# Performance work log

Measured on AMD Instinct MI355X. Metric: run time of the kernel, lower is better.

Reference implementation:

```python
import jax, jax.numpy as jnp
import numpy as np

EPS = 1e-5

def _inst_norm(x):
    # x: (B,C,H,W); torch .var(dim=2) is unbiased (ddof=1) over HW
    B, C, H, W = x.shape
    xf = x.reshape(B, C, H * W)
    mean = xf.mean(axis=2, keepdims=True)
    var = xf.var(axis=2, ddof=1, keepdims=True) + EPS
    return ((xf - mean) / jnp.sqrt(var)).reshape(B, C, H, W)

def _conv1x1(x, w, b):
    # (out,in) weight applied channelwise
    return jnp.einsum('oc,bchw->bohw', w, x) + b[None, :, None, None]

def setup_inputs() -> dict:
    key = jax.random.key(0)
    ks = jax.random.split(key, 10)
    B, C, H, W = 4, 512, 64, 64
    s = 1.0 / np.sqrt(C)
    return {
        'x_fcc': jax.random.normal(ks[0], (B, C, H, W), jnp.float32),
        'x_fss': jax.random.normal(ks[1], (B, C, H, W), jnp.float32),
        'w1': jax.random.normal(ks[2], (C, C), jnp.float32) * s,
        'b1': jax.random.normal(ks[3], (C,), jnp.float32) * 0.01,
        'w2': jax.random.normal(ks[4], (C, C), jnp.float32) * s,
        'b2': jax.random.normal(ks[5], (C,), jnp.float32) * 0.01,
        'w3': jax.random.normal(ks[6], (C, C), jnp.float32) * s,
        'b3': jax.random.normal(ks[7], (C,), jnp.float32) * 0.01,
        'wrs': jax.random.normal(ks[8], (C, C), jnp.float32) * s,
        'brs': jax.random.normal(ks[9], (C,), jnp.float32) * 0.01,
    }

def reference(x_fcc, x_fss, w1, b1, w2, b2, w3, b3, wrs, brs):
    Bc, Cc, Hc, Wc = x_fcc.shape
    Bs, Cs, Hs, Ws = x_fss.shape
    q = _conv1x1(_inst_norm(x_fcc), w1, b1).reshape(Bc, Cc, Hc * Wc)
    k = _conv1x1(_inst_norm(x_fss), w2, b2).reshape(Bs, Cs, Hs * Ws)
    v = _conv1x1(x_fss, w3, b3).reshape(Bc, Cs, Hs * Ws)
    # attention: (B, HWc, HWs), softmax over style positions
    scores = jnp.einsum('bcq,bck->bqk', q, k)
    A = jax.nn.softmax(scores, axis=-1)
    # aggregate style values per content position: (B, C, HWc)
    frs = jnp.einsum('bck,bqk->bcq', v, A).reshape(x_fcc.shape)
    frs = _conv1x1(frs, wrs, brs)
    return frs + x_fcc
```

## Files before the change

kernel.cpp:

```cpp
#include <hip/hip_runtime.h>
#include <hip/hip_bf16.h>


typedef _Float16 f16_t;
typedef _Float16 f16x8 __attribute__((ext_vector_type(8)));
typedef float f32x4 __attribute__((ext_vector_type(4)));

#define C_DIM 512
#define HW_DIM 4096
#define NBATCH 4
#define CHW (512L * 4096L)

__device__ inline f32x4 mfma_f16(f16x8 a, f16x8 b, f32x4 c) {
    return __builtin_amdgcn_mfma_f32_16x16x32_f16(a, b, c, 0, 0, 0);
}

__device__ inline void g2l16(const f16_t* g, f16_t* l) {
    auto gp = (const __attribute__((address_space(1))) uint32_t*)(uintptr_t)g;
    auto lp = (__attribute__((address_space(3))) uint32_t*)(uint32_t)(uintptr_t)l;
    __builtin_amdgcn_global_load_lds(gp, lp, 16, 0, 0);
}

template<int N> __device__ inline void vmwait() {
    static_assert(N == 0 || N == 6, "add vmcnt case");
    if constexpr (N == 0) asm volatile("s_waitcnt vmcnt(0)" ::: "memory");
    else                  asm volatile("s_waitcnt vmcnt(6)" ::: "memory");
}

__device__ inline void barrier_mem() {
    asm volatile("s_barrier" ::: "memory");
    __builtin_amdgcn_sched_barrier(0);
}

__global__ __launch_bounds__(256) void stats_kernel(
    const float* __restrict__ xc, const float* __restrict__ xs,
    float* __restrict__ meanc, float* __restrict__ rstdc,
    float* __restrict__ means, float* __restrict__ rstds)
{
    int id = blockIdx.x;
    int bc = id & 2047;
    const float4* x = (const float4*)((id < 2048 ? xc : xs) + (size_t)bc * HW_DIM);
    int tid = threadIdx.x;
    float s = 0.f, ss = 0.f;
#pragma unroll
    for (int i = 0; i < 4; i++) {
        float4 v = x[tid + (i << 8)];
        s += v.x + v.y + v.z + v.w;
        ss += v.x * v.x + v.y * v.y + v.z * v.z + v.w * v.w;
    }
#pragma unroll
    for (int o = 32; o; o >>= 1) { s += __shfl_down(s, o); ss += __shfl_down(ss, o); }
    __shared__ float red[8];
    if ((tid & 63) == 0) { red[(tid >> 6) * 2] = s; red[(tid >> 6) * 2 + 1] = ss; }
    __syncthreads();
    if (tid == 0) {
        s  = red[0] + red[2] + red[4] + red[6];
        ss = red[1] + red[3] + red[5] + red[7];
        float mean = s * (1.0f / 4096.0f);
        float var  = (ss - 4096.0f * mean * mean) * (1.0f / 4095.0f);
        float rstd = rsqrtf(var + 1e-5f);
        if (id < 2048) { meanc[bc] = mean; rstdc[bc] = rstd; }
        else           { means[bc] = mean; rstds[bc] = rstd; }
    }
}

__global__ __launch_bounds__(256) void pack_w4_kernel(
    const float* __restrict__ w0, const float* __restrict__ w1,
    const float* __restrict__ w2, const float* __restrict__ w3,
    f16_t* __restrict__ h0, f16_t* __restrict__ h1,
    f16_t* __restrict__ h2, f16_t* __restrict__ h3,
    const float* __restrict__ bb0, const float* __restrict__ bb1,
    const float* __restrict__ bb2, const float* __restrict__ bb3,
    float* __restrict__ biasws)
{
    int which = blockIdx.y;
    const float* w = which == 0 ? w0 : which == 1 ? w1 : which == 2 ? w2 : w3;
    f16_t* h = which == 0 ? h0 : which == 1 ? h1 : which == 2 ? h2 : h3;
    const float* bs = which == 0 ? bb0 : which == 1 ? bb1 : which == 2 ? bb2 : bb3;
    int i = blockIdx.x * 256 + threadIdx.x;
    h[i] = (f16_t)w[i];
    if (i < C_DIM) biasws[which * C_DIM + i] = bs[i];
}

__global__ __launch_bounds__(256) void pack_T_kernel(
    const float* __restrict__ xc, const float* __restrict__ xs,
    const float* __restrict__ meanc, const float* __restrict__ rstdc,
    const float* __restrict__ means, const float* __restrict__ rstds,
    f16_t* __restrict__ ch, f16_t* __restrict__ sh, f16_t* __restrict__ sraw)
{
    __shared__ float tile[32][33];
    int z = blockIdx.z;
    int b = z & 3, src = z >> 2;
    const float* x    = (src == 0) ? xc : xs;
    const float* mean = (src == 0) ? meanc : means;
    const float* rstd = (src == 0) ? rstdc : rstds;

    int c0 = blockIdx.y * 32, p0 = blockIdx.x * 32;
    int tp = threadIdx.x & 31, tc8 = threadIdx.x >> 5;
    const float* xb = x + ((size_t)b * C_DIM + c0) * HW_DIM + p0;
#pragma unroll
    for (int it = 0; it < 4; it++) {
        int c = tc8 + it * 8;
        tile[c][tp] = xb[(size_t)c * HW_DIM + tp];
    }
    __syncthreads();
    int wc = threadIdx.x & 31, wp8 = threadIdx.x >> 5;
    float m = mean[b * C_DIM + c0 + wc];
    float r = rstd[b * C_DIM + c0 + wc];
    size_t obase = ((size_t)b * HW_DIM + p0) * C_DIM + c0;
    f16_t* ohb = ((src == 0) ? ch : sh) + obase;
    f16_t* srb = sraw + obase;
#pragma unroll
    for (int it = 0; it < 4; it++) {
        int p = wp8 + it * 8;
        float v = tile[wc][p];
        ohb[(size_t)p * C_DIM + wc] = (f16_t)((v - m) * r);
        if (src == 1) srb[(size_t)p * C_DIM + wc] = (f16_t)v;
    }
}

__global__ __launch_bounds__(256) void softmax_rows(
    const float* __restrict__ S, f16_t* __restrict__ P)
{
    int row = blockIdx.x;
    int tid = threadIdx.x;
    int wave = tid >> 6, lane = tid & 63;
    const float4* sr = (const float4*)(S + (size_t)row * HW_DIM);
    float4 v[4];
    float mx = -3.4e38f;
#pragma unroll
    for (int i = 0; i < 4; i++) {
        v[i] = sr[tid + (i << 8)];
        mx = fmaxf(mx, fmaxf(fmaxf(v[i].x, v[i].y), fmaxf(v[i].z, v[i].w)));
    }
#pragma unroll
    for (int o = 32; o; o >>= 1) mx = fmaxf(mx, __shfl_down(mx, o));
    __shared__ float red[4];
    if (lane == 0) red[wave] = mx;
    __syncthreads();
    mx = fmaxf(fmaxf(red[0], red[1]), fmaxf(red[2], red[3]));
    float sum = 0.f;
#pragma unroll
    for (int i = 0; i < 4; i++) {
        v[i].x = __expf(v[i].x - mx); v[i].y = __expf(v[i].y - mx);
        v[i].z = __expf(v[i].z - mx); v[i].w = __expf(v[i].w - mx);
        sum += v[i].x + v[i].y + v[i].z + v[i].w;
    }
#pragma unroll
    for (int o = 32; o; o >>= 1) sum += __shfl_down(sum, o);
    __syncthreads();
    if (lane == 0) red[wave] = sum;
    __syncthreads();
    sum = red[0] + red[1] + red[2] + red[3];
    float inv = 1.0f / sum;
    uint2* pr = (uint2*)(P + (size_t)row * HW_DIM);
#pragma unroll
    for (int i = 0; i < 4; i++) {
        union { uint2 u; f16_t h[4]; } o;
        o.h[0] = (f16_t)(v[i].x * inv); o.h[1] = (f16_t)(v[i].y * inv);
        o.h[2] = (f16_t)(v[i].z * inv); o.h[3] = (f16_t)(v[i].w * inv);
        pr[tid + (i << 8)] = o.u;
    }
}

__global__ __launch_bounds__(256) void reduce4_kernel(
    const float* __restrict__ part, f16_t* __restrict__ out)
{
    size_t i = (size_t)blockIdx.x * 256 + threadIdx.x;
    const float4* p0 = (const float4*)part;
    const float4* p1 = (const float4*)(part + CHW);
    const float4* p2 = (const float4*)(part + 2 * CHW);
    const float4* p3 = (const float4*)(part + 3 * CHW);
    float4 a = p0[i], b = p1[i], c = p2[i], d = p3[i];
    union { uint2 u; f16_t h[4]; } o;
    o.h[0] = (f16_t)(a.x + b.x + c.x + d.x);
    o.h[1] = (f16_t)(a.y + b.y + c.y + d.y);
    o.h[2] = (f16_t)(a.z + b.z + c.z + d.z);
    o.h[3] = (f16_t)(a.w + b.w + c.w + d.w);
    ((uint2*)out)[i] = o.u;
}

template<int EPI, bool QK, int NT, int CHX, int CHY>
__global__ __launch_bounds__(512, 2) void gemm256(
    const f16_t* __restrict__ Ah, const f16_t* __restrict__ Bh,
    void* __restrict__ Cout0, const float* __restrict__ bias,
    const float* __restrict__ resid,
    int lda, int ldc,
    long sAz, long sBz, long sCz, long sRz, long sAw, long sBw, long sCw)
{
    constexpr int AE = 256 * 64;
    constexpr int BE = 128 * 64;
    constexpr int BUFE = AE + BE;
    __shared__ __align__(16) f16_t smem[3 * BUFE];

    int bx, by, bz;
    {
        const int nbx = gridDim.x, nby = gridDim.y, nbz = gridDim.z;
        const int lin = ((int)blockIdx.z * nby + blockIdx.y) * nbx + blockIdx.x;
        const int nwg = nbx * nby * nbz;
        const int cpx = nwg >> 3;
        const int logical = (lin & 7) * cpx + (lin >> 3);
        constexpr int CHB = CHX * CHY;
        const int chunk  = logical / CHB;
        const int within = logical % CHB;
        const int cx = within % CHX, cy = within / CHX;
        const int chunks_x = nbx / CHX;
        const int chx = chunk % chunks_x;
        int tt = chunk / chunks_x;
        const int chunks_y = nby / CHY;
        bz = tt / chunks_y;
        by = (tt % chunks_y) * CHY + cy;
        bx = chx * CHX + cx;
    }

    const int tid  = threadIdx.x;
    const int wave = tid >> 6, lane = tid & 63;
    const int wm = (wave >> 2) * 128;
    const int wn = (wave & 3) * 32;
    const int fr = lane & 15;
    const int g16 = lane >> 4;
    const int key = fr & 7;

    const int z   = QK ? (bz & 3) : bz;
    const int sel = QK ? (bz >> 2) : 0;
    const f16_t* Az = Ah + (size_t)z * sAz + (size_t)sel * sAw;
    const f16_t* Bz = Bh + (size_t)z * sBz + (size_t)sel * sBw;
    const float* biasp = bias ? (bias + (QK ? sel * C_DIM : 0)) : nullptr;
    const long mBlock = (long)by * 256;
    const long nBlock = (long)bx * 128;

    const int srow8 = lane >> 3;
    const int gsrc  = ((lane & 7) ^ srow8) * 8;
    const f16_t* aSrc[4]; const f16_t* bSrc[2];
    int aDst[4], bDst[2];
#pragma unroll
    for (int q = 0; q < 4; q++) {
        int j = 4 * wave + q;
        aSrc[q] = Az + (size_t)(mBlock + 8 * j + srow8) * lda + gsrc;
        aDst[q] = j * 512;
    }
#pragma unroll
    for (int q = 0; q < 2; q++) {
        int j = 2 * wave + q;
        bSrc[q] = Bz + (size_t)(nBlock + 8 * j + srow8) * lda + gsrc;
        bDst[q] = AE + j * 512;
    }

    auto stageA = [&](int t) {
        f16_t* dst = smem + (t % 3) * BUFE;
        const int k0 = t * 64;
#pragma unroll
        for (int q = 0; q < 4; q++) g2l16(aSrc[q] + k0, dst + aDst[q]);
    };
    auto stageB = [&](int t) {
        f16_t* dst = smem + (t % 3) * BUFE;
        const int k0 = t * 64;
#pragma unroll
        for (int q = 0; q < 2; q++) g2l16(bSrc[q] + k0, dst + bDst[q]);
    };

    f32x4 acc[8][2];
#pragma unroll
    for (int i = 0; i < 8; i++)
#pragma unroll
        for (int j = 0; j < 2; j++) acc[i][j] = (f32x4){0.f, 0.f, 0.f, 0.f};

    stageA(0); stageB(0); stageA(1); stageB(1);
    vmwait<6>();
    barrier_mem();

#pragma unroll
    for (int t = 0; t < NT; ++t) {
        const f16_t* buf = smem + (t % 3) * BUFE;
#pragma unroll
        for (int ks = 0; ks < 2; ++ks) {
            f16x8 a[8], b[2];
            const int gr = ((ks * 4 + g16) ^ key) * 8;
#pragma unroll
            for (int j2 = 0; j2 < 2; j2++)
                b[j2] = *reinterpret_cast<const f16x8*>(
                    buf + AE + (wn + j2 * 16 + fr) * 64 + gr);
#pragma unroll
            for (int mi = 0; mi < 8; mi++)
                a[mi] = *reinterpret_cast<const f16x8*>(
                    buf + (wm + mi * 16 + fr) * 64 + gr);
            if (t + 2 < NT) { if (ks == 0) stageA(t + 2); else stageB(t + 2); }
            if (ks == 1) {
                if (t + 2 < NT)      vmwait<6>();
                else if (t + 1 < NT) vmwait<0>();
            }
            barrier_mem();
            __builtin_amdgcn_s_setprio(1);
#pragma unroll
            for (int mi = 0; mi < 8; mi++)
#pragma unroll
                for (int j2 = 0; j2 < 2; j2++)
                    acc[mi][j2] = mfma_f16(a[mi], b[j2], acc[mi][j2]);
            __builtin_amdgcn_s_setprio(0);
            barrier_mem();
        }
    }

    const int col  = lane & 15;
    const int rowq = (lane >> 4) * 4;
    const size_t cbase = (size_t)z * sCz + (size_t)sel * sCw;
#pragma unroll
    for (int mi = 0; mi < 8; mi++) {
        const long mb = mBlock + wm + mi * 16 + rowq;
        float bv[4];
#pragma unroll
        for (int r = 0; r < 4; r++) bv[r] = biasp ? biasp[mb + r] : 0.0f;
#pragma unroll
        for (int j2 = 0; j2 < 2; j2++) {
            const long n = nBlock + wn + j2 * 16 + col;
            float v[4];
#pragma unroll
            for (int r = 0; r < 4; r++) v[r] = acc[mi][j2][r] + bv[r];
            if constexpr (EPI == 0) {
                float* O = (float*)Cout0 + cbase;
                const float* R = resid ? (resid + (size_t)z * sRz) : nullptr;
#pragma unroll
                for (int r = 0; r < 4; r++) {
                    size_t off = (size_t)(mb + r) * ldc + n;
                    O[off] = v[r] + (R ? R[off] : 0.0f);
                }
            } else if constexpr (EPI == 1) {
                f16_t* O = (f16_t*)Cout0 + cbase;
#pragma unroll
                for (int r = 0; r < 4; r++) O[(size_t)(mb + r) * ldc + n] = (f16_t)v[r];
            } else if constexpr (EPI == 3) {
                alignas(8) f16_t h[4];
#pragma unroll
                for (int r = 0; r < 4; r++) h[r] = (f16_t)v[r];
                *reinterpret_cast<uint2*>((f16_t*)Cout0 + cbase + (size_t)n * ldc + mb)
                    = *reinterpret_cast<uint2*>(h);
            } else {
                alignas(16) float h[4];
#pragma unroll
                for (int r = 0; r < 4; r++) h[r] = v[r];
                *reinterpret_cast<float4*>((float*)Cout0 + cbase + (size_t)n * ldc + mb)
                    = *reinterpret_cast<float4*>(h);
            }
        }
    }
}

extern "C" void kernel_launch(void* const* d_in, const int* in_sizes, int n_in,
                              void* d_out, int out_size, void* d_ws, size_t ws_size,
                              hipStream_t stream)
{
    const float* x_fcc = (const float*)d_in[0];
    const float* x_fss = (const float*)d_in[1];
    const float* w1 = (const float*)d_in[2];
    const float* b1 = (const float*)d_in[3];
    const float* w2 = (const float*)d_in[4];
    const float* b2 = (const float*)d_in[5];
    const float* w3 = (const float*)d_in[6];
    const float* b3 = (const float*)d_in[7];
    const float* wrs = (const float*)d_in[8];
    const float* brs = (const float*)d_in[9];
    float* out = (float*)d_out;
    (void)n_in; (void)in_sizes; (void)out_size; (void)ws_size;

    char* base = (char*)d_ws;
    size_t off = 0;
    auto take = [&](size_t bytes) -> char* {
        char* p = base + off;
        off += (bytes + 255) & ~(size_t)255;
        return p;
    };
    const size_t WB = (size_t)C_DIM * C_DIM * sizeof(f16_t);
    const size_t TB = (size_t)NBATCH * CHW * sizeof(f16_t);
    const long  TBe = NBATCH * CHW;

    float* meanc = (float*)take(2048 * 4);
    float* rstdc = (float*)take(2048 * 4);
    float* means = (float*)take(2048 * 4);
    float* rstds = (float*)take(2048 * 4);
    float* biasws = (float*)take(4 * C_DIM * 4);
    f16_t* w1h = (f16_t*)take(WB);
    f16_t* w2h = (f16_t*)take(WB);
    f16_t* w3h = (f16_t*)take(WB);
    f16_t* wrh = (f16_t*)take(WB);
    f16_t* qT = (f16_t*)take(TB);
    f16_t* kT = (f16_t*)take(TB);
    f16_t* vh   = (f16_t*)take(TB);
    f16_t* frsT = (f16_t*)take(TB);
    char* packb = take(8 * TB);
    f16_t* xcT  = (f16_t*)(packb);
    f16_t* xsT  = (f16_t*)(packb + TB);
    f16_t* xsrT = (f16_t*)(packb + 2 * TB);
    float* Smat = (float*)(packb);
    f16_t* Pmat = (f16_t*)(packb + 4 * TB);
    float* Part = (float*)(packb + 6 * TB);

    dim3 blk(256);
    dim3 blk5(512);

    stats_kernel<<<dim3(4096), blk, 0, stream>>>(x_fcc, x_fss, meanc, rstdc, means, rstds);
    pack_w4_kernel<<<dim3(1024, 4), blk, 0, stream>>>(
        w1, w2, w3, wrs, w1h, w2h, w3h, wrh, b1, b2, b3, brs, biasws);
    pack_T_kernel<<<dim3(128, 16, 8), blk, 0, stream>>>(
        x_fcc, x_fss, meanc, rstdc, means, rstds, xcT, xsT, xsrT);
    gemm256<3, true, 8, 8, 2><<<dim3(32, 2, 8), blk5, 0, stream>>>(
        w1h, xcT, qT, biasws, nullptr, C_DIM, C_DIM,
        0L, CHW, CHW, 0L, (long)C_DIM * C_DIM, TBe, TBe);
    gemm256<1, false, 8, 8, 2><<<dim3(32, 2, 4), blk5, 0, stream>>>(
        w3h, xsrT, vh, biasws + 2 * C_DIM, nullptr, C_DIM, HW_DIM,
        0L, CHW, CHW, 0L, 0L, 0L, 0L);
    for (int b = 0; b < NBATCH; b++) {
        gemm256<0, false, 8, 8, 4><<<dim3(32, 16, 1), blk5, 0, stream>>>(
            qT + (size_t)b * CHW, kT + (size_t)b * CHW,
            Smat, nullptr, nullptr, C_DIM, HW_DIM,
            0L, 0L, 0L, 0L, 0L, 0L, 0L);
        softmax_rows<<<dim3(4096), blk, 0, stream>>>(Smat, Pmat);
        gemm256<4, false, 16, 8, 2><<<dim3(32, 2, 4), blk5, 0, stream>>>(
            vh + (size_t)b * CHW, Pmat,
            Part, nullptr, nullptr, HW_DIM, C_DIM,
            1024L, 1024L, CHW, 0L, 0L, 0L, 0L);
        reduce4_kernel<<<dim3(CHW / 1024), blk, 0, stream>>>(
            Part, frsT + (size_t)b * CHW);
    }
    gemm256<0, false, 8, 8, 2><<<dim3(32, 2, 4), blk5, 0, stream>>>(
        wrh, frsT, out, biasws + 3 * C_DIM, x_fcc, C_DIM, HW_DIM,
        0L, CHW, CHW, CHW, 0L, 0L, 0L);
}
```

Measured before the change: 533.4 us.

## Enlarge GEMM tile to 256x256 with double-buffered split-unit LDS staging

The GEMM kernel's output tile grows from 256x128 to 256x256. Each wave now computes 128x64 with 32 accumulators, and all launch grids are halved in x. The shared-memory pipeline changes from a 3-stage ring to a 2-stage double buffer split into four 128-row units, with finer-grained staging interleaved across half-steps. The aim is more MFMA work per byte loaded and fewer blocks, at the cost of more registers (which may cut occupancy below 2 blocks/CU), less pipeline depth, and fewer workgroups on the small GEMMs.

```diff
diff --git a/kernel.cpp b/kernel.cpp
--- a/kernel.cpp
+++ b/kernel.cpp
@@ -22,9 +22,9 @@
 }
 
 template<int N> __device__ inline void vmwait() {
-    static_assert(N == 0 || N == 6, "add vmcnt case");
+    static_assert(N == 0 || N == 2, "add vmcnt case");
     if constexpr (N == 0) asm volatile("s_waitcnt vmcnt(0)" ::: "memory");
-    else                  asm volatile("s_waitcnt vmcnt(6)" ::: "memory");
+    else                  asm volatile("s_waitcnt vmcnt(2)" ::: "memory");
 }
 
 __device__ inline void barrier_mem() {
@@ -188,10 +188,8 @@
     int lda, int ldc,
     long sAz, long sBz, long sCz, long sRz, long sAw, long sBw, long sCw)
 {
-    constexpr int AE = 256 * 64;
-    constexpr int BE = 128 * 64;
-    constexpr int BUFE = AE + BE;
-    __shared__ __align__(16) f16_t smem[3 * BUFE];
+    constexpr int UNIT = 128 * 64;
+    __shared__ __align__(16) f16_t smem[8 * UNIT];
 
     int bx, by, bz;
     {
@@ -216,10 +214,13 @@
     const int tid  = threadIdx.x;
     const int wave = tid >> 6, lane = tid & 63;
     const int wm = (wave >> 2) * 128;
-    const int wn = (wave & 3) * 32;
+    const int wn = (wave & 3) * 64;
     const int fr = lane & 15;
     const int g16 = lane >> 4;
     const int key = fr & 7;
+    const int ha  = wave >> 2;
+    const int hb  = wn >> 7;
+    const int rB  = wn - hb * 128;
 
     const int z   = QK ? (bz & 3) : bz;
     const int sel = QK ? (bz >> 2) : 0;
@@ -227,75 +228,84 @@
     const f16_t* Bz = Bh + (size_t)z * sBz + (size_t)sel * sBw;
     const float* biasp = bias ? (bias + (QK ? sel * C_DIM : 0)) : nullptr;
     const long mBlock = (long)by * 256;
-    const long nBlock = (long)bx * 128;
+    const long nBlock = (long)bx * 256;
 
     const int srow8 = lane >> 3;
     const int gsrc  = ((lane & 7) ^ srow8) * 8;
-    const f16_t* aSrc[4]; const f16_t* bSrc[2];
-    int aDst[4], bDst[2];
-#pragma unroll
-    for (int q = 0; q < 4; q++) {
-        int j = 4 * wave + q;
-        aSrc[q] = Az + (size_t)(mBlock + 8 * j + srow8) * lda + gsrc;
-        aDst[q] = j * 512;
-    }
-#pragma unroll
-    for (int q = 0; q < 2; q++) {
-        int j = 2 * wave + q;
-        bSrc[q] = Bz + (size_t)(nBlock + 8 * j + srow8) * lda + gsrc;
-        bDst[q] = AE + j * 512;
-    }
-
-    auto stageA = [&](int t) {
-        f16_t* dst = smem + (t % 3) * BUFE;
-        const int k0 = t * 64;
-#pragma unroll
-        for (int q = 0; q < 4; q++) g2l16(aSrc[q] + k0, dst + aDst[q]);
+    const f16_t* aRow[2][2]; const f16_t* bRow[2][2];
+#pragma unroll
+    for (int h = 0; h < 2; h++)
+#pragma unroll
+        for (int q = 0; q < 2; q++) {
+            long r = q * 64 + wave * 8 + srow8;
+            aRow[h][q] = Az + (size_t)(mBlock + h * 128 + r) * lda + gsrc;
+            bRow[h][q] = Bz + (size_t)(nBlock + h * 128 + r) * lda + gsrc;
+        }
+    const int dst0 = wave * 512;
+    const int dst1 = 4096 + wave * 512;
+
+    auto stageU = [&](int t, int isB, int h) {
+        f16_t* ub = smem + ((t & 1) * 4 + isB * 2 + h) * UNIT;
+        const long k0 = (long)t * 64;
+        if (isB) {
+            g2l16(bRow[h][0] + k0, ub + dst0);
+            g2l16(bRow[h][1] + k0, ub + dst1);
+        } else {
+            g2l16(aRow[h][0] + k0, ub + dst0);
+            g2l16(aRow[h][1] + k0, ub + dst1);
+        }
     };
-    auto stageB = [&](int t) {
-        f16_t* dst = smem + (t % 3) * BUFE;
-        const int k0 = t * 64;
-#pragma unroll
-        for (int q = 0; q < 2; q++) g2l16(bSrc[q] + k0, dst + bDst[q]);
-    };
-
-    f32x4 acc[8][2];
+
+    f32x4 acc[8][4];
 #pragma unroll
     for (int i = 0; i < 8; i++)
 #pragma unroll
-        for (int j = 0; j < 2; j++) acc[i][j] = (f32x4){0.f, 0.f, 0.f, 0.f};
-
-    stageA(0); stageB(0); stageA(1); stageB(1);
-    vmwait<6>();
+        for (int j = 0; j < 4; j++) acc[i][j] = (f32x4){0.f, 0.f, 0.f, 0.f};
+
+    stageU(0, 0, 0); stageU(0, 0, 1); stageU(0, 1, 0); stageU(0, 1, 1);
+    if (NT > 1) stageU(1, 0, 0);
+    vmwait<2>();
     barrier_mem();
 
 #pragma unroll
     for (int t = 0; t < NT; ++t) {
-        const f16_t* buf = smem + (t % 3) * BUFE;
+        const f16_t* bufA = smem + ((t & 1) * 4 + ha) * UNIT;
+        const f16_t* bufB = smem + ((t & 1) * 4 + 2 + hb) * UNIT;
 #pragma unroll
         for (int ks = 0; ks < 2; ++ks) {
-            f16x8 a[8], b[2];
             const int gr = ((ks * 4 + g16) ^ key) * 8;
-#pragma unroll
-            for (int j2 = 0; j2 < 2; j2++)
-                b[j2] = *reinterpret_cast<const f16x8*>(
-                    buf + AE + (wn + j2 * 16 + fr) * 64 + gr);
+            f16x8 a[8], b0, b1;
 #pragma unroll
             for (int mi = 0; mi < 8; mi++)
                 a[mi] = *reinterpret_cast<const f16x8*>(
-                    buf + (wm + mi * 16 + fr) * 64 + gr);
-            if (t + 2 < NT) { if (ks == 0) stageA(t + 2); else stageB(t + 2); }
-            if (ks == 1) {
-                if (t + 2 < NT)      vmwait<6>();
+                    bufA + (mi * 16 + fr) * 64 + gr);
+            b0 = *reinterpret_cast<const f16x8*>(bufB + (rB + fr) * 64 + gr);
+            b1 = *reinterpret_cast<const f16x8*>(bufB + (rB + 16 + fr) * 64 + gr);
+            if (ks == 0) { if (t + 1 < NT) stageU(t + 1, 0, 1); }
+            else         { if (t + 1 < NT) stageU(t + 1, 1, 1); }
+            barrier_mem();
+            __builtin_amdgcn_s_setprio(1);
+#pragma unroll
+            for (int mi = 0; mi < 8; mi++) {
+                acc[mi][0] = mfma_f16(a[mi], b0, acc[mi][0]);
+                acc[mi][1] = mfma_f16(a[mi], b1, acc[mi][1]);
+            }
+            __builtin_amdgcn_s_setprio(0);
+            barrier_mem();
+            b0 = *reinterpret_cast<const f16x8*>(bufB + (rB + 32 + fr) * 64 + gr);
+            b1 = *reinterpret_cast<const f16x8*>(bufB + (rB + 48 + fr) * 64 + gr);
+            if (ks == 0) { if (t + 1 < NT) stageU(t + 1, 1, 0); }
+            else {
+                if (t + 2 < NT) { stageU(t + 2, 0, 0); vmwait<2>(); }
                 else if (t + 1 < NT) vmwait<0>();
             }
             barrier_mem();
             __builtin_amdgcn_s_setprio(1);
 #pragma unroll
-            for (int mi = 0; mi < 8; mi++)
-#pragma unroll
-                for (int j2 = 0; j2 < 2; j2++)
-                    acc[mi][j2] = mfma_f16(a[mi], b[j2], acc[mi][j2]);
+            for (int mi = 0; mi < 8; mi++) {
+                acc[mi][2] = mfma_f16(a[mi], b0, acc[mi][2]);
+                acc[mi][3] = mfma_f16(a[mi], b1, acc[mi][3]);
+            }
             __builtin_amdgcn_s_setprio(0);
             barrier_mem();
         }
@@ -311,7 +321,7 @@
 #pragma unroll
         for (int r = 0; r < 4; r++) bv[r] = biasp ? biasp[mb + r] : 0.0f;
 #pragma unroll
-        for (int j2 = 0; j2 < 2; j2++) {
+        for (int j2 = 0; j2 < 4; j2++) {
             const long n = nBlock + wn + j2 * 16 + col;
             float v[4];
 #pragma unroll
@@ -402,26 +412,26 @@
         w1, w2, w3, wrs, w1h, w2h, w3h, wrh, b1, b2, b3, brs, biasws);
     pack_T_kernel<<<dim3(128, 16, 8), blk, 0, stream>>>(
         x_fcc, x_fss, meanc, rstdc, means, rstds, xcT, xsT, xsrT);
-    gemm256<3, true, 8, 8, 2><<<dim3(32, 2, 8), blk5, 0, stream>>>(
+    gemm256<3, true, 8, 8, 2><<<dim3(16, 2, 8), blk5, 0, stream>>>(
         w1h, xcT, qT, biasws, nullptr, C_DIM, C_DIM,
         0L, CHW, CHW, 0L, (long)C_DIM * C_DIM, TBe, TBe);
-    gemm256<1, false, 8, 8, 2><<<dim3(32, 2, 4), blk5, 0, stream>>>(
+    gemm256<1, false, 8, 8, 2><<<dim3(16, 2, 4), blk5, 0, stream>>>(
         w3h, xsrT, vh, biasws + 2 * C_DIM, nullptr, C_DIM, HW_DIM,
         0L, CHW, CHW, 0L, 0L, 0L, 0L);
     for (int b = 0; b < NBATCH; b++) {
-        gemm256<0, false, 8, 8, 4><<<dim3(32, 16, 1), blk5, 0, stream>>>(
+        gemm256<0, false, 8, 4, 8><<<dim3(16, 16, 1), blk5, 0, stream>>>(
             qT + (size_t)b * CHW, kT + (size_t)b * CHW,
             Smat, nullptr, nullptr, C_DIM, HW_DIM,
             0L, 0L, 0L, 0L, 0L, 0L, 0L);
         softmax_rows<<<dim3(4096), blk, 0, stream>>>(Smat, Pmat);
-        gemm256<4, false, 16, 8, 2><<<dim3(32, 2, 4), blk5, 0, stream>>>(
+        gemm256<4, false, 16, 8, 2><<<dim3(16, 2, 4), blk5, 0, stream>>>(
             vh + (size_t)b * CHW, Pmat,
             Part, nullptr, nullptr, HW_DIM, C_DIM,
             1024L, 1024L, CHW, 0L, 0L, 0L, 0L);
         reduce4_kernel<<<dim3(CHW / 1024), blk, 0, stream>>>(
             Part, frsT + (size_t)b * CHW);
     }
-    gemm256<0, false, 8, 8, 2><<<dim3(32, 2, 4), blk5, 0, stream>>>(
+    gemm256<0, false, 8, 8, 2><<<dim3(16, 2, 4), blk5, 0, stream>>>(
         wrh, frsT, out, biasws + 3 * C_DIM, x_fcc, C_DIM, HW_DIM,
         0L, CHW, CHW, CHW, 0L, 0L, 0L);
 }
```

New measurement: 599.5 us. 1.12x slower.

## Replace 256x128 triple-buffered GEMM with 128x128 double-buffered 256-thread kernel

Applied to the files above, without the earlier changes.

Swaps the 512-thread, 256x128-tile GEMM with three-stage, K=64 LDS pipelining for a 256-thread 128x128 tile using K=32 steps and a double buffer. Each wave now computes a 64x64 subtile. All GEMM launches double their grid in M and their K-step counts. The smaller tile and smaller LDS footprint raise occupancy and block count. In exchange there is less data reuse per tile and a shallower prefetch, with a full vmcnt(0) wait and barrier every step, which may expose load latency.

```diff
diff --git a/kernel.cpp b/kernel.cpp
--- a/kernel.cpp
+++ b/kernel.cpp
@@ -21,15 +21,33 @@
     __builtin_amdgcn_global_load_lds(gp, lp, 16, 0, 0);
 }
 
-template<int N> __device__ inline void vmwait() {
-    static_assert(N == 0 || N == 6, "add vmcnt case");
-    if constexpr (N == 0) asm volatile("s_waitcnt vmcnt(0)" ::: "memory");
-    else                  asm volatile("s_waitcnt vmcnt(6)" ::: "memory");
+__device__ inline void vmwait0() {
+    asm volatile("s_waitcnt vmcnt(0)" ::: "memory");
 }
 
 __device__ inline void barrier_mem() {
     asm volatile("s_barrier" ::: "memory");
     __builtin_amdgcn_sched_barrier(0);
+}
+
+template<int CHX, int CHY>
+__device__ inline void xcd_swizzle(int& bx, int& by, int& bz) {
+    const int nbx = gridDim.x, nby = gridDim.y, nbz = gridDim.z;
+    const int lin = ((int)blockIdx.z * nby + blockIdx.y) * nbx + blockIdx.x;
+    const int nwg = nbx * nby * nbz;
+    const int cpx = nwg >> 3;
+    const int logical = (lin & 7) * cpx + (lin >> 3);
+    constexpr int CHB = CHX * CHY;
+    const int chunk  = logical / CHB;
+    const int within = logical % CHB;
+    const int cx = within % CHX, cy = within / CHX;
+    const int chunks_x = nbx / CHX;
+    const int chx = chunk % chunks_x;
+    int tt = chunk / chunks_x;
+    const int chunks_y = nby / CHY;
+    bz = tt / chunks_y;
+    by = (tt % chunks_y) * CHY + cy;
+    bx = chx * CHX + cx;
 }
 
 __global__ __launch_bounds__(256) void stats_kernel(
@@ -181,122 +199,88 @@
 }
 
 template<int EPI, bool QK, int NT, int CHX, int CHY>
-__global__ __launch_bounds__(512, 2) void gemm256(
+__global__ __launch_bounds__(256, 4) void gemm128c(
     const f16_t* __restrict__ Ah, const f16_t* __restrict__ Bh,
     void* __restrict__ Cout0, const float* __restrict__ bias,
     const float* __restrict__ resid,
     int lda, int ldc,
     long sAz, long sBz, long sCz, long sRz, long sAw, long sBw, long sCw)
 {
-    constexpr int AE = 256 * 64;
-    constexpr int BE = 128 * 64;
-    constexpr int BUFE = AE + BE;
-    __shared__ __align__(16) f16_t smem[3 * BUFE];
+    constexpr int BUFE = 256 * 32;
+    __shared__ __align__(16) f16_t smem[2 * BUFE];
 
     int bx, by, bz;
-    {
-        const int nbx = gridDim.x, nby = gridDim.y, nbz = gridDim.z;
-        const int lin = ((int)blockIdx.z * nby + blockIdx.y) * nbx + blockIdx.x;
-        const int nwg = nbx * nby * nbz;
-        const int cpx = nwg >> 3;
-        const int logical = (lin & 7) * cpx + (lin >> 3);
-        constexpr int CHB = CHX * CHY;
-        const int chunk  = logical / CHB;
-        const int within = logical % CHB;
-        const int cx = within % CHX, cy = within / CHX;
-        const int chunks_x = nbx / CHX;
-        const int chx = chunk % chunks_x;
-        int tt = chunk / chunks_x;
-        const int chunks_y = nby / CHY;
-        bz = tt / chunks_y;
-        by = (tt % chunks_y) * CHY + cy;
-        bx = chx * CHX + cx;
-    }
+    xcd_swizzle<CHX, CHY>(bx, by, bz);
 
     const int tid  = threadIdx.x;
     const int wave = tid >> 6, lane = tid & 63;
-    const int wm = (wave >> 2) * 128;
-    const int wn = (wave & 3) * 32;
+    const int wm = (wave >> 1) * 64;
+    const int wn = (wave & 1) * 64;
     const int fr = lane & 15;
     const int g16 = lane >> 4;
-    const int key = fr & 7;
+    const int key = fr & 3;
 
     const int z   = QK ? (bz & 3) : bz;
     const int sel = QK ? (bz >> 2) : 0;
     const f16_t* Az = Ah + (size_t)z * sAz + (size_t)sel * sAw;
     const f16_t* Bz = Bh + (size_t)z * sBz + (size_t)sel * sBw;
     const float* biasp = bias ? (bias + (QK ? sel * C_DIM : 0)) : nullptr;
-    const long mBlock = (long)by * 256;
+    const long mBlock = (long)by * 128;
     const long nBlock = (long)bx * 128;
 
-    const int srow8 = lane >> 3;
-    const int gsrc  = ((lane & 7) ^ srow8) * 8;
-    const f16_t* aSrc[4]; const f16_t* bSrc[2];
-    int aDst[4], bDst[2];
-#pragma unroll
-    for (int q = 0; q < 4; q++) {
-        int j = 4 * wave + q;
-        aSrc[q] = Az + (size_t)(mBlock + 8 * j + srow8) * lda + gsrc;
+    const int srow4 = lane >> 2;
+    const int gsrc  = ((lane & 3) ^ (srow4 & 3)) * 8;
+    const f16_t* aSrc[2]; const f16_t* bSrc[2];
+    int aDst[2], bDst[2];
+#pragma unroll
+    for (int q = 0; q < 2; q++) {
+        int j = wave + q * 4;
+        aSrc[q] = Az + (size_t)(mBlock + 16 * j + srow4) * lda + gsrc;
         aDst[q] = j * 512;
-    }
-#pragma unroll
-    for (int q = 0; q < 2; q++) {
-        int j = 2 * wave + q;
-        bSrc[q] = Bz + (size_t)(nBlock + 8 * j + srow8) * lda + gsrc;
-        bDst[q] = AE + j * 512;
-    }
-
-    auto stageA = [&](int t) {
-        f16_t* dst = smem + (t % 3) * BUFE;
-        const int k0 = t * 64;
-#pragma unroll
-        for (int q = 0; q < 4; q++) g2l16(aSrc[q] + k0, dst + aDst[q]);
-    };
-    auto stageB = [&](int t) {
-        f16_t* dst = smem + (t % 3) * BUFE;
-        const int k0 = t * 64;
+        bSrc[q] = Bz + (size_t)(nBlock + 16 * j + srow4) * lda + gsrc;
+        bDst[q] = 4096 + j * 512;
+    }
+
+    auto stage = [&](int t) {
+        f16_t* dst = smem + (t & 1) * BUFE;
+        const int k0 = t * 32;
+#pragma unroll
+        for (int q = 0; q < 2; q++) g2l16(aSrc[q] + k0, dst + aDst[q]);
 #pragma unroll
         for (int q = 0; q < 2; q++) g2l16(bSrc[q] + k0, dst + bDst[q]);
     };
 
-    f32x4 acc[8][2];
-#pragma unroll
-    for (int i = 0; i < 8; i++)
-#pragma unroll
-        for (int j = 0; j < 2; j++) acc[i][j] = (f32x4){0.f, 0.f, 0.f, 0.f};
-
-    stageA(0); stageB(0); stageA(1); stageB(1);
-    vmwait<6>();
+    f32x4 acc[4][4];
+#pragma unroll
+    for (int i = 0; i < 4; i++)
+#pragma unroll
+        for (int j = 0; j < 4; j++) acc[i][j] = (f32x4){0.f, 0.f, 0.f, 0.f};
+
+    stage(0);
+    vmwait0();
     barrier_mem();
 
+    const int gr = (g16 ^ key) * 8;
 #pragma unroll
     for (int t = 0; t < NT; ++t) {
-        const f16_t* buf = smem + (t % 3) * BUFE;
-#pragma unroll
-        for (int ks = 0; ks < 2; ++ks) {
-            f16x8 a[8], b[2];
-            const int gr = ((ks * 4 + g16) ^ key) * 8;
-#pragma unroll
-            for (int j2 = 0; j2 < 2; j2++)
-                b[j2] = *reinterpret_cast<const f16x8*>(
-                    buf + AE + (wn + j2 * 16 + fr) * 64 + gr);
-#pragma unroll
-            for (int mi = 0; mi < 8; mi++)
-                a[mi] = *reinterpret_cast<const f16x8*>(
-                    buf + (wm + mi * 16 + fr) * 64 + gr);
-            if (t + 2 < NT) { if (ks == 0) stageA(t + 2); else stageB(t + 2); }
-            if (ks == 1) {
-                if (t + 2 < NT)      vmwait<6>();
-                else if (t + 1 < NT) vmwait<0>();
-            }
-            barrier_mem();
-            __builtin_amdgcn_s_setprio(1);
-#pragma unroll
-            for (int mi = 0; mi < 8; mi++)
-#pragma unroll
-                for (int j2 = 0; j2 < 2; j2++)
-                    acc[mi][j2] = mfma_f16(a[mi], b[j2], acc[mi][j2]);
-            __builtin_amdgcn_s_setprio(0);
+        if (t + 1 < NT) stage(t + 1);
+        const f16_t* buf = smem + (t & 1) * BUFE;
+        f16x8 a[4], b[4];
+#pragma unroll
+        for (int mi = 0; mi < 4; mi++)
+            a[mi] = *reinterpret_cast<const f16x8*>(
+                buf + (wm + mi * 16 + fr) * 32 + gr);
+#pragma unroll
+        for (int j2 = 0; j2 < 4; j2++)
+            b[j2] = *reinterpret_cast<const f16x8*>(
+                buf + 4096 + (wn + j2 * 16 + fr) * 32 + gr);
+#pragma unroll
+        for (int mi = 0; mi < 4; mi++)
+#pragma unroll
+            for (int j2 = 0; j2 < 4; j2++)
+                acc[mi][j2] = mfma_f16(a[mi], b[j2], acc[mi][j2]);
+        if (t + 1 < NT) {
+            vmwait0();
             barrier_mem();
         }
     }
@@ -305,13 +289,13 @@
     const int rowq = (lane >> 4) * 4;
     const size_t cbase = (size_t)z * sCz + (size_t)sel * sCw;
 #pragma unroll
-    for (int mi = 0; mi < 8; mi++) {
+    for (int mi = 0; mi < 4; mi++) {
         const long mb = mBlock + wm + mi * 16 + rowq;
         float bv[4];
 #pragma unroll
         for (int r = 0; r < 4; r++) bv[r] = biasp ? biasp[mb + r] : 0.0f;
 #pragma unroll
-        for (int j2 = 0; j2 < 2; j2++) {
+        for (int j2 = 0; j2 < 4; j2++) {
             const long n = nBlock + wn + j2 * 16 + col;
             float v[4];
 #pragma unroll
@@ -395,33 +379,32 @@
     float* Part = (float*)(packb + 6 * TB);
 
     dim3 blk(256);
-    dim3 blk5(512);
 
     stats_kernel<<<dim3(4096), blk, 0, stream>>>(x_fcc, x_fss, meanc, rstdc, means, rstds);
     pack_w4_kernel<<<dim3(1024, 4), blk, 0, stream>>>(
         w1, w2, w3, wrs, w1h, w2h, w3h, wrh, b1, b2, b3, brs, biasws);
     pack_T_kernel<<<dim3(128, 16, 8), blk, 0, stream>>>(
         x_fcc, x_fss, meanc, rstdc, means, rstds, xcT, xsT, xsrT);
-    gemm256<3, true, 8, 8, 2><<<dim3(32, 2, 8), blk5, 0, stream>>>(
+    gemm128c<3, true, 16, 16, 2><<<dim3(32, 4, 8), blk, 0, stream>>>(
         w1h, xcT, qT, biasws, nullptr, C_DIM, C_DIM,
         0L, CHW, CHW, 0L, (long)C_DIM * C_DIM, TBe, TBe);
-    gemm256<1, false, 8, 8, 2><<<dim3(32, 2, 4), blk5, 0, stream>>>(
+    gemm128c<1, false, 16, 16, 2><<<dim3(32, 4, 4), blk, 0, stream>>>(
         w3h, xsrT, vh, biasws + 2 * C_DIM, nullptr, C_DIM, HW_DIM,
         0L, CHW, CHW, 0L, 0L, 0L, 0L);
     for (int b = 0; b < NBATCH; b++) {
-        gemm256<0, false, 8, 8, 4><<<dim3(32, 16, 1), blk5, 0, stream>>>(
+        gemm128c<0, false, 16, 8, 4><<<dim3(32, 32, 1), blk, 0, stream>>>(
             qT + (size_t)b * CHW, kT + (size_t)b * CHW,
             Smat, nullptr, nullptr, C_DIM, HW_DIM,
             0L, 0L, 0L, 0L, 0L, 0L, 0L);
         softmax_rows<<<dim3(4096), blk, 0, stream>>>(Smat, Pmat);
-        gemm256<4, false, 16, 8, 2><<<dim3(32, 2, 4), blk5, 0, stream>>>(
+        gemm128c<4, false, 32, 8, 2><<<dim3(32, 4, 4), blk, 0, stream>>>(
             vh + (size_t)b * CHW, Pmat,
             Part, nullptr, nullptr, HW_DIM, C_DIM,
             1024L, 1024L, CHW, 0L, 0L, 0L, 0L);
         reduce4_kernel<<<dim3(CHW / 1024), blk, 0, stream>>>(
             Part, frsT + (size_t)b * CHW);
     }
-    gemm256<0, false, 8, 8, 2><<<dim3(32, 2, 4), blk5, 0, stream>>>(
+    gemm128c<0, false, 16, 16, 2><<<dim3(32, 4, 4), blk, 0, stream>>>(
         wrh, frsT, out, biasws + 3 * C_DIM, x_fcc, C_DIM, HW_DIM,
         0L, CHW, CHW, CHW, 0L, 0L, 0L);
 }
```

Result: no change. 539.1 us (+1.1%).
